# Kernel optimization log

Hardware: AMD Instinct MI355X
Metric: run time of the kernel (lower is better)

## Reference

```python
import jax, jax.numpy as jnp
from jax import lax
import numpy as np

DIM = 192
NH = 6
HEAD = DIM // NH
SCALE = HEAD ** -0.5
WS = (2, 7, 7)
NW = WS[0] * WS[1] * WS[2]  # 98 tokens per window
HID = 4 * DIM
EPS = 1e-5


def _rel_index():
    # static relative-position index, computed once in numpy
    cd, ch, cw = [np.arange(s) for s in WS]
    coords = np.stack(np.meshgrid(cd, ch, cw, indexing='ij')).reshape(3, -1)  # [3, NW]
    rel = coords[:, :, None] - coords[:, None, :]          # [3, NW, NW]
    rel = rel.transpose(1, 2, 0) + np.array([WS[0] - 1, WS[1] - 1, WS[2] - 1])
    rel[:, :, 0] *= (2 * WS[1] - 1) * (2 * WS[2] - 1)
    rel[:, :, 1] *= (2 * WS[2] - 1)
    return jnp.asarray(rel.sum(-1))                         # [NW, NW] int32

REL_IDX = _rel_index()


def _ln(x, g, b):
    mu = jnp.mean(x, -1, keepdims=True)
    var = jnp.mean(jnp.square(x - mu), -1, keepdims=True)
    return (x - mu) * lax.rsqrt(var + EPS) * g + b


def setup_inputs() -> dict:
    key = jax.random.key(0)
    ks = jax.random.split(key, 10)
    B, D, H, W = 2, 16, 56, 56
    N = D * H * W
    s = 0.02
    return {
        'x': jax.random.normal(ks[0], (B, N, DIM), jnp.float32),
        'norm1_g': jnp.ones((DIM,), jnp.float32),
        'norm1_b': jnp.zeros((DIM,), jnp.float32),
        'qkv_w': jax.random.normal(ks[1], (DIM, 3 * DIM), jnp.float32) * s,
        'qkv_b': jnp.zeros((3 * DIM,), jnp.float32),
        'bias_table': jax.random.normal(ks[2], ((2 * WS[0] - 1) * (2 * WS[1] - 1) * (2 * WS[2] - 1), NH), jnp.float32) * s,
        'proj_w': jax.random.normal(ks[3], (DIM, DIM), jnp.float32) * s,
        'proj_b': jnp.zeros((DIM,), jnp.float32),
        'norm2_g': jnp.ones((DIM,), jnp.float32),
        'norm2_b': jnp.zeros((DIM,), jnp.float32),
        'fc1_w': jax.random.normal(ks[4], (DIM, HID), jnp.float32) * s,
        'fc1_b': jnp.zeros((HID,), jnp.float32),
        'dw_w': jax.random.normal(ks[5], (HID, 1, 3, 3, 3), jnp.float32) * s,  # OIDHW depthwise
        'dw_b': jnp.zeros((HID,), jnp.float32),
        'fc2_w': jax.random.normal(ks[6], (HID, DIM), jnp.float32) * s,
        'fc2_b': jnp.zeros((DIM,), jnp.float32),
        'D': D, 'H': H, 'W': W,
    }


def reference(x, norm1_g, norm1_b, qkv_w, qkv_b, bias_table, proj_w, proj_b,
              norm2_g, norm2_b, fc1_w, fc1_b, dw_w, dw_b, fc2_w, fc2_b, D, H, W):
    B, N, C = x.shape
    Wd, Wh, Ww = WS
    nd, nh, nw = D // Wd, H // Wh, W // Ww

    # --- windowed attention branch ---
    h = _ln(x, norm1_g, norm1_b).reshape(B, D, H, W, C)
    h = h.reshape(B, nd, Wd, nh, Wh, nw, Ww, C)
    h = h.transpose(0, 1, 3, 5, 2, 4, 6, 7).reshape(-1, NW, C)  # [Bw, NW, C]
    Bw = h.shape[0]

    qkv = (h @ qkv_w + qkv_b).reshape(Bw, NW, 3, NH, HEAD)
    qkv = qkv.transpose(2, 0, 3, 1, 4)                           # [3, Bw, NH, NW, HEAD]
    q, k, v = qkv[0] * SCALE, qkv[1], qkv[2]

    attn = jnp.einsum('bhnd,bhmd->bhnm', q, k)                   # [Bw, NH, NW, NW]
    rel_bias = bias_table[REL_IDX]                               # [NW, NW, NH]
    attn = attn + rel_bias.transpose(2, 0, 1)[None]
    attn = jax.nn.softmax(attn, axis=-1)

    o = jnp.einsum('bhnm,bhmd->bhnd', attn, v)                   # [Bw, NH, NW, HEAD]
    o = o.transpose(0, 2, 1, 3).reshape(Bw, NW, C)
    o = o @ proj_w + proj_b

    # window reverse
    o = o.reshape(B, nd, nh, nw, Wd, Wh, Ww, C)
    o = o.transpose(0, 1, 4, 2, 5, 3, 6, 7).reshape(B, N, C)

    x = x + 0.5 * o  # DropPath scale_residual=0.5 in eval

    # --- MixFFN3D branch ---
    h = _ln(x, norm2_g, norm2_b)
    h = h @ fc1_w + fc1_b                                        # [B, N, HID]
    h = h.transpose(0, 2, 1).reshape(B, HID, D, H, W)
    h = lax.conv_general_dilated(
        h, dw_w, window_strides=(1, 1, 1), padding=[(1, 1)] * 3,
        dimension_numbers=('NCDHW', 'OIDHW', 'NCDHW'),
        feature_group_count=HID) + dw_b[None, :, None, None, None]
    h = h.reshape(B, HID, N).transpose(0, 2, 1)
    h = jax.nn.gelu(h, approximate=False)
    h = h @ fc2_w + fc2_b

    return x + 0.5 * h
```

## Files before the change

kernel.cpp:

```cpp
#include <hip/hip_runtime.h>
#include <hip/hip_bf16.h>

typedef unsigned short u16;
typedef unsigned int   u32;
typedef __bf16 bf16x8 __attribute__((ext_vector_type(8)));
typedef float  f32x4  __attribute__((ext_vector_type(4)));
typedef float  f32x2  __attribute__((ext_vector_type(2)));

#define M_TOK 100352
#define M_HALF 50176
#define DIMC  192
#define HIDC  768
#define SCALE_F 0.17677669529663688f

__device__ __forceinline__ float b2f(u16 u) {
    u32 x = ((u32)u) << 16; float f; __builtin_memcpy(&f, &x, 4); return f;
}
__device__ __forceinline__ u16 f2b(float f) {
    u32 x; __builtin_memcpy(&x, &f, 4);
    x = x + 0x7FFFu + ((x >> 16) & 1u);
    return (u16)(x >> 16);
}
__device__ __forceinline__ float lo2f(u32 w) {
    u32 x = w << 16; float f; __builtin_memcpy(&f, &x, 4); return f;
}
__device__ __forceinline__ float hi2f(u32 w) {
    u32 x = w & 0xFFFF0000u; float f; __builtin_memcpy(&f, &x, 4); return f;
}
__device__ __forceinline__ void g2l16(const u16* g, u16* l) {
    __builtin_amdgcn_global_load_lds(
        (const __attribute__((address_space(1))) u32*)g,
        (__attribute__((address_space(3))) u32*)l, 16, 0, 0);
}

__global__ __launch_bounds__(256) void prep_weights(
    const float* __restrict__ qkv_w, const float* __restrict__ proj_w,
    const float* __restrict__ fc1_w, const float* __restrict__ fc2_w,
    const float* __restrict__ dw_w,
    u16* __restrict__ qkvt, u16* __restrict__ projt, u16* __restrict__ fc1t,
    u16* __restrict__ fc2t, float* __restrict__ dwtf)
{
    int id = blockIdx.x * 256 + threadIdx.x;
    if (id < 110592)      { int n = id / 192, k = id % 192;                 qkvt[id] = f2b(qkv_w[k * 576 + n]); }
    else if (id < 147456) { int e = id - 110592, n = e / 192, k = e % 192;  projt[e] = f2b(proj_w[k * 192 + n]); }
    else if (id < 294912) { int e = id - 147456, n = e / 192, k = e % 192;  fc1t[e]  = f2b(fc1_w[k * 768 + n]); }
    else if (id < 442368) { int e = id - 294912, n = e / 768, k = e % 768;  fc2t[e]  = f2b(fc2_w[k * 192 + n]); }
    else if (id < 463104) { int e = id - 442368, t = e / 768, c = e % 768;  dwtf[e]  = dw_w[c * 27 + t]; }
}

__global__ __launch_bounds__(256) void biasmat_kernel(
    const float* __restrict__ btab, float* __restrict__ bmat)
{
    int id = blockIdx.x * 256 + threadIdx.x;
    if (id >= 6 * 112 * 112) return;
    int h = id / 12544, rem = id % 12544, i = rem / 112, j = rem % 112;
    float v;
    if (j >= 98)      v = -1e30f;
    else if (i >= 98) v = 0.0f;
    else {
        int di = i / 49, hi = (i / 7) % 7, wi = i % 7;
        int dj = j / 49, hj = (j / 7) % 7, wj = j % 7;
        int idx = (di - dj + 1) * 169 + (hi - hj + 6) * 13 + (wi - wj + 6);
        v = btab[idx * 6 + h];
    }
    bmat[id] = v;
}

template<bool PERM, bool BF_IN>
__global__ __launch_bounds__(256) void ln_kernel(
    const void* __restrict__ xin, const float* __restrict__ g,
    const float* __restrict__ bb, u16* __restrict__ out)
{
    int row  = blockIdx.x * 4 + (threadIdx.x >> 6);
    int lane = threadIdx.x & 63;
    float v0, v1, v2;
    if (BF_IN) {
        const u16* xr = (const u16*)xin + (size_t)row * DIMC;
        v0 = b2f(xr[lane]); v1 = b2f(xr[lane + 64]); v2 = b2f(xr[lane + 128]);
    } else {
        const float* xr = (const float*)xin + (size_t)row * DIMC;
        v0 = xr[lane]; v1 = xr[lane + 64]; v2 = xr[lane + 128];
    }
    float s  = v0 + v1 + v2;
    float s2 = v0 * v0 + v1 * v1 + v2 * v2;
    #pragma unroll
    for (int m = 1; m < 64; m <<= 1) { s += __shfl_xor(s, m); s2 += __shfl_xor(s2, m); }
    float mu = s * (1.0f / 192.0f);
    float rs = rsqrtf(s2 * (1.0f / 192.0f) - mu * mu + 1e-5f);
    size_t ob;
    if (PERM) {
        int b = row / 50176, r = row % 50176;
        int d = r / 3136, r2 = r % 3136, h = r2 / 56, w = r2 % 56;
        int widx = ((b * 8 + (d >> 1)) * 8 + h / 7) * 8 + w / 7;
        int tok  = (d & 1) * 49 + (h % 7) * 7 + (w % 7);
        ob = ((size_t)widx * 98 + tok) * DIMC;
    } else {
        ob = (size_t)row * DIMC;
    }
    out[ob + lane]       = f2b((v0 - mu) * rs * g[lane]       + bb[lane]);
    out[ob + lane + 64]  = f2b((v1 - mu) * rs * g[lane + 64]  + bb[lane + 64]);
    out[ob + lane + 128] = f2b((v2 - mu) * rs * g[lane + 128] + bb[lane + 128]);
}

template<int EPI>
__global__ __launch_bounds__(256) void gemm_bt(
    const u16* __restrict__ A, const u16* __restrict__ Bt,
    const float* __restrict__ bias, int K, int N, int NBN,
    u16* __restrict__ outb, const float* __restrict__ xres,
    u16* __restrict__ x2b, float* __restrict__ outf, int mofs)
{
    __shared__ __align__(16) u16 Alds[128 * 32];
    __shared__ __align__(16) u16 Blds[64 * 32];
    int bid = blockIdx.x;
    int cpx = gridDim.x >> 3;
    int swz = (bid & 7) * cpx + (bid >> 3);
    int m0 = (swz / NBN) * 128;
    int n0 = (swz % NBN) * 64;
    int t  = threadIdx.x;
    int ar = t >> 2, ac = (t & 3) * 8;
    int lane = t & 63, wid = t >> 6;
    int wm = wid >> 1, wn = wid & 1;
    int lrow = lane & 15, lko = (lane >> 4) * 8;
    const u16* Ag  = A  + (size_t)(m0 + ar) * K + ac;
    const u16* Ag2 = Ag + (size_t)64 * K;
    const u16* Bg  = Bt + (size_t)(n0 + ar) * K + ac;
    u16* lA  = Alds + t * 8;
    u16* lA2 = Alds + 2048 + t * 8;
    u16* lB  = Blds + t * 8;
    f32x4 acc[4][2] = {};
    for (int kt = 0; kt < K; kt += 32) {
        __syncthreads();
        g2l16(Ag  + kt, lA);
        g2l16(Ag2 + kt, lA2);
        g2l16(Bg  + kt, lB);
        __syncthreads();
        bf16x8 af[4], bfr[2];
        #pragma unroll
        for (int mi = 0; mi < 4; mi++)
            af[mi] = *(const bf16x8*)&Alds[(wm * 64 + mi * 16 + lrow) * 32 + lko];
        #pragma unroll
        for (int ni = 0; ni < 2; ni++)
            bfr[ni] = *(const bf16x8*)&Blds[(wn * 32 + ni * 16 + lrow) * 32 + lko];
        #pragma unroll
        for (int mi = 0; mi < 4; mi++)
            #pragma unroll
            for (int ni = 0; ni < 2; ni++)
                acc[mi][ni] = __builtin_amdgcn_mfma_f32_16x16x32_bf16(af[mi], bfr[ni], acc[mi][ni], 0, 0, 0);
    }
    int r0 = (lane >> 4) * 4, cl = lane & 15;
    #pragma unroll
    for (int ni = 0; ni < 2; ni++) {
        int col = n0 + wn * 32 + ni * 16 + cl;
        float bv = bias[col];
        #pragma unroll
        for (int mi = 0; mi < 4; mi++) {
            #pragma unroll
            for (int r = 0; r < 4; r++) {
                int row = m0 + wm * 64 + mi * 16 + r0 + r;
                float v = acc[mi][ni][r] + bv;
                if (EPI == 0) {
                    outb[(size_t)row * N + col] = f2b(v);
                } else if (EPI == 1) {
                    int widx = row / 98, tok = row % 98;
                    int b = widx >> 9, rem = widx & 511;
                    int bd = rem >> 6, bh = (rem >> 3) & 7, bw = rem & 7;
                    int td = tok / 49, rr = tok % 49, th = rr / 7, tw = rr % 7;
                    int d = bd * 2 + td, h = bh * 7 + th, w = bw * 7 + tw;
                    size_t gg = ((size_t)b * 50176 + (d * 56 + h) * 56 + w) * (size_t)N + col;
                    x2b[gg] = f2b(xres[gg] + 0.5f * v);
                } else {
                    size_t gg = (size_t)(row + mofs) * N + col;
                    outf[gg] = b2f(x2b[gg]) + 0.5f * v;
                }
            }
        }
    }
}

__global__ __launch_bounds__(64) void attn_mfma_kernel(
    const u16* __restrict__ qkv, const float* __restrict__ bmat,
    u16* __restrict__ outb)
{
    __shared__ __align__(16) u16 Klds[112 * 40];
    __shared__ __align__(16) u16 Vt[32 * 136];
    __shared__ __align__(16) u16 Plds[16 * 136];
    int widx = blockIdx.x, head = blockIdx.y;
    int l = threadIdx.x;
    int c = l & 15, g = l >> 4;
    size_t wbase = (size_t)widx * (98 * 576) + head * 32;

    for (int e = l; e < 448; e += 64) {
        int rr = e >> 2, seg = (e & 3) * 8;
        uint4 kr = {0, 0, 0, 0}, vr = {0, 0, 0, 0};
        if (rr < 98) {
            kr = *(const uint4*)(qkv + wbase + (size_t)rr * 576 + 192 + seg);
            vr = *(const uint4*)(qkv + wbase + (size_t)rr * 576 + 384 + seg);
        }
        *(uint4*)&Klds[rr * 40 + seg] = kr;
        int sw = ((seg >> 3) & 3) << 4;
        int pc = rr ^ sw;
        const u16* vp = (const u16*)&vr;
        #pragma unroll
        for (int u = 0; u < 8; u++)
            Vt[(seg + u) * 136 + pc] = vp[u];
    }
    {
        int d = l >> 1, half = l & 1;
        int sw = ((d >> 3) & 3) << 4;
        uint4 z = {0, 0, 0, 0};
        *(uint4*)&Vt[d * 136 + ((112 + 8 * half) ^ sw)] = z;
        if (l < 32) {
            int i = l >> 1; half = l & 1;
            int swp = ((i >> 2) & 3) << 4;
            *(uint4*)&Plds[i * 136 + ((112 + 8 * half) ^ swp)] = z;
        }
    }

    for (int it = 0; it < 7; ++it) {
        int qtok = 16 * it + c; if (qtok > 97) qtok = 97;
        bf16x8 qf = *(const bf16x8*)(qkv + wbase + (size_t)qtok * 576 + g * 8);
        f32x4 s[7];
        f32x4 z = {};
        #pragma unroll
        for (int jt = 0; jt < 7; ++jt) {
            bf16x8 kf = *(const bf16x8*)&Klds[(16 * jt + c) * 40 + g * 8];
            s[jt] = __builtin_amdgcn_mfma_f32_16x16x32_bf16(qf, kf, z, 0, 0, 0);
        }
        const float* bb = bmat + ((size_t)head * 112 + 16 * it + 4 * g) * 112 + c;
        float sm[4];
        #pragma unroll
        for (int r = 0; r < 4; ++r) {
            float m = -1e30f;
            #pragma unroll
            for (int jt = 0; jt < 7; ++jt) {
                float v = s[jt][r] * SCALE_F + bb[r * 112 + 16 * jt];
                s[jt][r] = v;
                m = fmaxf(m, v);
            }
            m = fmaxf(m, __shfl_xor(m, 1)); m = fmaxf(m, __shfl_xor(m, 2));
            m = fmaxf(m, __shfl_xor(m, 4)); m = fmaxf(m, __shfl_xor(m, 8));
            float su = 0.f;
            #pragma unroll
            for (int jt = 0; jt < 7; ++jt) {
                float p = __expf(s[jt][r] - m);
                s[jt][r] = p;
                su += p;
            }
            su += __shfl_xor(su, 1); su += __shfl_xor(su, 2);
            su += __shfl_xor(su, 4); su += __shfl_xor(su, 8);
            sm[r] = su;
        }
        #pragma unroll
        for (int r = 0; r < 4; ++r) {
            int prow = 4 * g + r;
            int swp = ((prow >> 2) & 3) << 4;
            #pragma unroll
            for (int jt = 0; jt < 7; ++jt)
                Plds[prow * 136 + ((16 * jt + c) ^ swp)] = f2b(s[jt][r]);
        }
        bf16x8 pa[4];
        int swr = ((c >> 2) & 3) << 4;
        #pragma unroll
        for (int ks = 0; ks < 4; ++ks)
            pa[ks] = *(const bf16x8*)&Plds[c * 136 + ((32 * ks + 8 * g) ^ swr)];
        #pragma unroll
        for (int dt = 0; dt < 2; ++dt) {
            f32x4 o = {};
            int vrow = 16 * dt + c;
            int swv = ((vrow >> 3) & 3) << 4;
            #pragma unroll
            for (int ks = 0; ks < 4; ++ks) {
                bf16x8 vb = *(const bf16x8*)&Vt[vrow * 136 + ((32 * ks + 8 * g) ^ swv)];
                o = __builtin_amdgcn_mfma_f32_16x16x32_bf16(pa[ks], vb, o, 0, 0, 0);
            }
            #pragma unroll
            for (int r = 0; r < 4; ++r) {
                int row = 16 * it + 4 * g + r;
                if (row < 98)
                    outb[((size_t)widx * 98 + row) * DIMC + head * 32 + 16 * dt + c]
                        = f2b(o[r] / sm[r]);
            }
        }
    }
}

__global__ __launch_bounds__(256, 8) void dwconv_gelu_kernel(
    const u16* __restrict__ hid, const float* __restrict__ dwtf,
    const float* __restrict__ dwb, u16* __restrict__ outb)
{
    int bid = blockIdx.x;
    int swz = (bid & 7) * 1176 + (bid >> 3);
    int gid = swz * 256 + threadIdx.x;
    int cg = gid % 192;
    int t  = gid / 192;
    int d  = t & 15;
    t >>= 4;
    int wg = t % 14;
    int h  = t / 14;
    int w0 = wg * 4;
    int c0 = cg * 4;

    f32x2 acc[4][2];
    {
        float4 bv = *(const float4*)(dwb + c0);
        #pragma unroll
        for (int wi = 0; wi < 4; ++wi) {
            acc[wi][0] = f32x2{bv.x, bv.y};
            acc[wi][1] = f32x2{bv.z, bv.w};
        }
    }

    #pragma unroll
    for (int iz = 0; iz < 3; ++iz) {
        int zz = d - 1 + iz;
        if ((unsigned)zz >= 16u) continue;
        #pragma unroll
        for (int iy = 0; iy < 3; ++iy) {
            int yy = h - 1 + iy;
            if ((unsigned)yy >= 56u) continue;
            uint2 raw[6];
            const u16* rp = hid + ((size_t)(zz * 56 + yy) * 56 + w0 - 1) * HIDC + c0;
            #pragma unroll
            for (int ix = 0; ix < 6; ++ix) {
                uint2 iv = {0, 0};
                if ((unsigned)(w0 - 1 + ix) < 56u)
                    iv = *(const uint2*)(rp + (size_t)ix * HIDC);
                raw[ix] = iv;
            }
            const float* wrow = dwtf + (size_t)(iz * 9 + iy * 3) * HIDC + c0;
            float4 wv0 = *(const float4*)(wrow);
            float4 wv1 = *(const float4*)(wrow + HIDC);
            float4 wv2 = *(const float4*)(wrow + 2 * HIDC);
            f32x2 wp[3][2] = {
                { f32x2{wv0.x, wv0.y}, f32x2{wv0.z, wv0.w} },
                { f32x2{wv1.x, wv1.y}, f32x2{wv1.z, wv1.w} },
                { f32x2{wv2.x, wv2.y}, f32x2{wv2.z, wv2.w} } };
            #pragma unroll
            for (int p = 0; p < 6; ++p) {
                f32x2 i0 = f32x2{lo2f(raw[p].x), hi2f(raw[p].x)};
                f32x2 i1 = f32x2{lo2f(raw[p].y), hi2f(raw[p].y)};
                #pragma unroll
                for (int dx = 0; dx < 3; ++dx) {
                    if (dx > p || dx < p - 3) continue;
                    acc[p - dx][0] += i0 * wp[dx][0];
                    acc[p - dx][1] += i1 * wp[dx][1];
                }
            }
        }
    }

    size_t tok0 = (size_t)(d * 56 + h) * 56 + w0;
    #pragma unroll
    for (int wi = 0; wi < 4; ++wi) {
        u16 res[4];
        #pragma unroll
        for (int pr = 0; pr < 2; ++pr) {
            #pragma unroll
            for (int u = 0; u < 2; ++u) {
                float a = acc[wi][pr][u];
                float tt = a * (1.5957691216f + 0.0713548162f * a * a);
                res[pr * 2 + u] = f2b(a / (1.0f + __expf(-tt)));
            }
        }
        uint2 ov;
        ov.x = (u32)res[0] | ((u32)res[1] << 16);
        ov.y = (u32)res[2] | ((u32)res[3] << 16);
        *(uint2*)(outb + (tok0 + wi) * HIDC + c0) = ov;
    }
}

extern "C" void kernel_launch(void* const* d_in, const int* in_sizes, int n_in,
                              void* d_out, int out_size, void* d_ws, size_t ws_size,
                              hipStream_t stream)
{
    const float* x      = (const float*)d_in[0];
    const float* n1g    = (const float*)d_in[1];
    const float* n1b    = (const float*)d_in[2];
    const float* qkv_w  = (const float*)d_in[3];
    const float* qkv_b  = (const float*)d_in[4];
    const float* btab   = (const float*)d_in[5];
    const float* proj_w = (const float*)d_in[6];
    const float* proj_b = (const float*)d_in[7];
    const float* n2g    = (const float*)d_in[8];
    const float* n2b    = (const float*)d_in[9];
    const float* fc1_w  = (const float*)d_in[10];
    const float* fc1_b  = (const float*)d_in[11];
    const float* dw_w   = (const float*)d_in[12];
    const float* dw_b   = (const float*)d_in[13];
    const float* fc2_w  = (const float*)d_in[14];
    const float* fc2_b  = (const float*)d_in[15];

    char* ws = (char*)d_ws;
    u16*   qkvt  = (u16*)(ws);
    u16*   projt = (u16*)(ws + 221184);
    u16*   fc1t  = (u16*)(ws + 294912);
    u16*   fc2t  = (u16*)(ws + 589824);
    float* dwtf  = (float*)(ws + 884736);
    u16*   r1    = (u16*)(ws + 1160192);
    u16*   qkvb  = (u16*)(ws + 39695360LL);
    u16*   x2b   = (u16*)(ws + 39695360LL);
    u16*   hid_c = (u16*)(ws + 78230528LL);
    float* bmat  = (float*)(ws + 155300864LL);
    u16*   gelu_c= (u16*)(ws + 155300864LL);

    prep_weights<<<dim3(1809), dim3(256), 0, stream>>>(qkv_w, proj_w, fc1_w, fc2_w, dw_w,
                                                       qkvt, projt, fc1t, fc2t, dwtf);
    biasmat_kernel<<<dim3(294), dim3(256), 0, stream>>>(btab, bmat);
    ln_kernel<true, false><<<dim3(25088), dim3(256), 0, stream>>>(x, n1g, n1b, r1);
    gemm_bt<0><<<dim3(7056), dim3(256), 0, stream>>>(r1, qkvt, qkv_b, 192, 576, 9,
                                                     qkvb, nullptr, nullptr, nullptr, 0);
    attn_mfma_kernel<<<dim3(1024, 6), dim3(64), 0, stream>>>(qkvb, bmat, r1);
    gemm_bt<1><<<dim3(2352), dim3(256), 0, stream>>>(r1, projt, proj_b, 192, 192, 3,
                                                     nullptr, x, x2b, nullptr, 0);
    ln_kernel<false, true><<<dim3(25088), dim3(256), 0, stream>>>(x2b, n2g, n2b, r1);
    for (int b = 0; b < 2; b++) {
        const u16* h2c = r1 + (size_t)b * M_HALF * DIMC;
        gemm_bt<0><<<dim3(4704), dim3(256), 0, stream>>>(h2c, fc1t, fc1_b, 192, 768, 12,
                                                         hid_c, nullptr, nullptr, nullptr, 0);
        dwconv_gelu_kernel<<<dim3(9408), dim3(256), 0, stream>>>(hid_c, dwtf, dw_b, gelu_c);
        gemm_bt<2><<<dim3(1176), dim3(256), 0, stream>>>(gelu_c, fc2t, fc2_b, 768, 192, 3,
                                                         nullptr, nullptr, x2b, (float*)d_out,
                                                         b * M_HALF);
    }
}
```

Before: 728.9 us.

## Split dwconv into interior/edge kernels and double GEMM k-step per sync

The GEMM loop now loads 64 K-columns per iteration (two 32-wide LDS slices) and runs two MFMA sub-steps between barriers, halving the number of __syncthreads per tile. The depthwise conv+GELU is split into an interior kernel with all boundary checks removed and a separate edge kernel that keeps the checks for boundary tokens. This trims barrier and branch overhead at the cost of doubled LDS use in the GEMM and an extra launch. The GEMM change assumes K is a multiple of 64, which holds for 192 and 768.

```diff
diff --git a/kernel.cpp b/kernel.cpp
--- a/kernel.cpp
+++ b/kernel.cpp
@@ -109,43 +109,47 @@
     u16* __restrict__ outb, const float* __restrict__ xres,
     u16* __restrict__ x2b, float* __restrict__ outf, int mofs)
 {
-    __shared__ __align__(16) u16 Alds[128 * 32];
-    __shared__ __align__(16) u16 Blds[64 * 32];
+    __shared__ __align__(16) u16 Alds[2 * 128 * 32];
+    __shared__ __align__(16) u16 Blds[2 * 64 * 32];
     int bid = blockIdx.x;
     int cpx = gridDim.x >> 3;
     int swz = (bid & 7) * cpx + (bid >> 3);
     int m0 = (swz / NBN) * 128;
     int n0 = (swz % NBN) * 64;
     int t  = threadIdx.x;
-    int ar = t >> 2, ac = (t & 3) * 8;
     int lane = t & 63, wid = t >> 6;
     int wm = wid >> 1, wn = wid & 1;
     int lrow = lane & 15, lko = (lane >> 4) * 8;
-    const u16* Ag  = A  + (size_t)(m0 + ar) * K + ac;
-    const u16* Ag2 = Ag + (size_t)64 * K;
-    const u16* Bg  = Bt + (size_t)(n0 + ar) * K + ac;
-    u16* lA  = Alds + t * 8;
-    u16* lA2 = Alds + 2048 + t * 8;
-    u16* lB  = Blds + t * 8;
+    int sr = t >> 2, sc = (t & 3) * 8;
+    const u16* Ag = A  + (size_t)(m0 + sr) * K + sc;
+    const u16* Bg = Bt + (size_t)(n0 + sr) * K + sc;
+    u16* lA = Alds + t * 8;
+    u16* lB = Blds + t * 8;
     f32x4 acc[4][2] = {};
-    for (int kt = 0; kt < K; kt += 32) {
+    for (int kt = 0; kt < K; kt += 64) {
         __syncthreads();
-        g2l16(Ag  + kt, lA);
-        g2l16(Ag2 + kt, lA2);
-        g2l16(Bg  + kt, lB);
+        g2l16(Ag + kt,                    lA);
+        g2l16(Ag + (size_t)64 * K + kt,   lA + 2048);
+        g2l16(Ag + kt + 32,               lA + 4096);
+        g2l16(Ag + (size_t)64 * K + kt + 32, lA + 6144);
+        g2l16(Bg + kt,      lB);
+        g2l16(Bg + kt + 32, lB + 2048);
         __syncthreads();
-        bf16x8 af[4], bfr[2];
-        #pragma unroll
-        for (int mi = 0; mi < 4; mi++)
-            af[mi] = *(const bf16x8*)&Alds[(wm * 64 + mi * 16 + lrow) * 32 + lko];
-        #pragma unroll
-        for (int ni = 0; ni < 2; ni++)
-            bfr[ni] = *(const bf16x8*)&Blds[(wn * 32 + ni * 16 + lrow) * 32 + lko];
-        #pragma unroll
-        for (int mi = 0; mi < 4; mi++)
+        #pragma unroll
+        for (int kk = 0; kk < 2; ++kk) {
+            bf16x8 af[4], bfr[2];
+            #pragma unroll
+            for (int mi = 0; mi < 4; mi++)
+                af[mi] = *(const bf16x8*)&Alds[kk * 4096 + (wm * 64 + mi * 16 + lrow) * 32 + lko];
             #pragma unroll
             for (int ni = 0; ni < 2; ni++)
-                acc[mi][ni] = __builtin_amdgcn_mfma_f32_16x16x32_bf16(af[mi], bfr[ni], acc[mi][ni], 0, 0, 0);
+                bfr[ni] = *(const bf16x8*)&Blds[kk * 2048 + (wn * 32 + ni * 16 + lrow) * 32 + lko];
+            #pragma unroll
+            for (int mi = 0; mi < 4; mi++)
+                #pragma unroll
+                for (int ni = 0; ni < 2; ni++)
+                    acc[mi][ni] = __builtin_amdgcn_mfma_f32_16x16x32_bf16(af[mi], bfr[ni], acc[mi][ni], 0, 0, 0);
+        }
     }
     int r0 = (lane >> 4) * 4, cl = lane & 15;
     #pragma unroll
@@ -284,20 +288,21 @@
     }
 }
 
-__global__ __launch_bounds__(256, 8) void dwconv_gelu_kernel(
+__global__ __launch_bounds__(256, 8) void dwconv_gelu_int(
     const u16* __restrict__ hid, const float* __restrict__ dwtf,
     const float* __restrict__ dwb, u16* __restrict__ outb)
 {
     int bid = blockIdx.x;
-    int swz = (bid & 7) * 1176 + (bid >> 3);
+    int xcd = bid & 7, lin = bid >> 3;
+    int swz = (xcd < 4 ? xcd * 851 : 3404 + (xcd - 4) * 850) + lin;
     int gid = swz * 256 + threadIdx.x;
     int cg = gid % 192;
-    int t  = gid / 192;
-    int d  = t & 15;
-    t >>= 4;
-    int wg = t % 14;
-    int h  = t / 14;
-    int w0 = wg * 4;
+    int iu = gid / 192;
+    int d  = iu % 14 + 1;
+    int r  = iu / 14;
+    int wg = r % 12;
+    int h  = r / 12 + 1;
+    int w0 = wg * 4 + 4;
     int c0 = cg * 4;
 
     f32x2 acc[4][2];
@@ -310,24 +315,18 @@
         }
     }
 
+    const u16* rp0 = hid + (((size_t)(d - 1) * 56 + (h - 1)) * 56 + (w0 - 1)) * HIDC + c0;
+    const float* wb0 = dwtf + c0;
     #pragma unroll
     for (int iz = 0; iz < 3; ++iz) {
-        int zz = d - 1 + iz;
-        if ((unsigned)zz >= 16u) continue;
         #pragma unroll
         for (int iy = 0; iy < 3; ++iy) {
-            int yy = h - 1 + iy;
-            if ((unsigned)yy >= 56u) continue;
+            const u16* rp = rp0 + (size_t)(iz * 3136 + iy * 56) * HIDC;
             uint2 raw[6];
-            const u16* rp = hid + ((size_t)(zz * 56 + yy) * 56 + w0 - 1) * HIDC + c0;
-            #pragma unroll
-            for (int ix = 0; ix < 6; ++ix) {
-                uint2 iv = {0, 0};
-                if ((unsigned)(w0 - 1 + ix) < 56u)
-                    iv = *(const uint2*)(rp + (size_t)ix * HIDC);
-                raw[ix] = iv;
-            }
-            const float* wrow = dwtf + (size_t)(iz * 9 + iy * 3) * HIDC + c0;
+            #pragma unroll
+            for (int ix = 0; ix < 6; ++ix)
+                raw[ix] = *(const uint2*)(rp + (size_t)ix * HIDC);
+            const float* wrow = wb0 + (size_t)(iz * 9 + iy * 3) * HIDC;
             float4 wv0 = *(const float4*)(wrow);
             float4 wv1 = *(const float4*)(wrow + HIDC);
             float4 wv2 = *(const float4*)(wrow + 2 * HIDC);
@@ -354,14 +353,95 @@
     for (int wi = 0; wi < 4; ++wi) {
         u16 res[4];
         #pragma unroll
-        for (int pr = 0; pr < 2; ++pr) {
+        for (int pr = 0; pr < 2; ++pr)
             #pragma unroll
             for (int u = 0; u < 2; ++u) {
                 float a = acc[wi][pr][u];
                 float tt = a * (1.5957691216f + 0.0713548162f * a * a);
                 res[pr * 2 + u] = f2b(a / (1.0f + __expf(-tt)));
             }
-        }
+        uint2 ov;
+        ov.x = (u32)res[0] | ((u32)res[1] << 16);
+        ov.y = (u32)res[2] | ((u32)res[3] << 16);
+        *(uint2*)(outb + (tok0 + wi) * HIDC + c0) = ov;
+    }
+}
+
+__global__ __launch_bounds__(256, 8) void dwconv_gelu_edge(
+    const u16* __restrict__ hid, const float* __restrict__ dwtf,
+    const float* __restrict__ dwb, u16* __restrict__ outb)
+{
+    int gid = blockIdx.x * 256 + threadIdx.x;
+    int cg = gid % 192;
+    int u  = gid / 192;
+    int d, h, wg;
+    if (u < 1568)      { d = (u < 784) ? 0 : 15; int rr = u % 784; h = rr / 14; wg = rr % 14; }
+    else if (u < 1960) { int rr = u - 1568; h = (rr < 196) ? 0 : 55; rr %= 196; d = 1 + rr / 14; wg = rr % 14; }
+    else               { int rr = u - 1960; wg = (rr < 756) ? 0 : 13; rr %= 756; d = 1 + rr / 54; h = 1 + rr % 54; }
+    int w0 = wg * 4;
+    int c0 = cg * 4;
+
+    f32x2 acc[4][2];
+    {
+        float4 bv = *(const float4*)(dwb + c0);
+        #pragma unroll
+        for (int wi = 0; wi < 4; ++wi) {
+            acc[wi][0] = f32x2{bv.x, bv.y};
+            acc[wi][1] = f32x2{bv.z, bv.w};
+        }
+    }
+
+    #pragma unroll
+    for (int iz = 0; iz < 3; ++iz) {
+        int zz = d - 1 + iz;
+        if ((unsigned)zz >= 16u) continue;
+        #pragma unroll
+        for (int iy = 0; iy < 3; ++iy) {
+            int yy = h - 1 + iy;
+            if ((unsigned)yy >= 56u) continue;
+            uint2 raw[6];
+            const u16* rp = hid + ((size_t)(zz * 56 + yy) * 56 + w0 - 1) * HIDC + c0;
+            #pragma unroll
+            for (int ix = 0; ix < 6; ++ix) {
+                uint2 iv = {0, 0};
+                if ((unsigned)(w0 - 1 + ix) < 56u)
+                    iv = *(const uint2*)(rp + (size_t)ix * HIDC);
+                raw[ix] = iv;
+            }
+            const float* wrow = dwtf + (size_t)(iz * 9 + iy * 3) * HIDC + c0;
+            float4 wv0 = *(const float4*)(wrow);
+            float4 wv1 = *(const float4*)(wrow + HIDC);
+            float4 wv2 = *(const float4*)(wrow + 2 * HIDC);
+            f32x2 wp[3][2] = {
+                { f32x2{wv0.x, wv0.y}, f32x2{wv0.z, wv0.w} },
+                { f32x2{wv1.x, wv1.y}, f32x2{wv1.z, wv1.w} },
+                { f32x2{wv2.x, wv2.y}, f32x2{wv2.z, wv2.w} } };
+            #pragma unroll
+            for (int p = 0; p < 6; ++p) {
+                f32x2 i0 = f32x2{lo2f(raw[p].x), hi2f(raw[p].x)};
+                f32x2 i1 = f32x2{lo2f(raw[p].y), hi2f(raw[p].y)};
+                #pragma unroll
+                for (int dx = 0; dx < 3; ++dx) {
+                    if (dx > p || dx < p - 3) continue;
+                    acc[p - dx][0] += i0 * wp[dx][0];
+                    acc[p - dx][1] += i1 * wp[dx][1];
+                }
+            }
+        }
+    }
+
+    size_t tok0 = (size_t)(d * 56 + h) * 56 + w0;
+    #pragma unroll
+    for (int wi = 0; wi < 4; ++wi) {
+        u16 res[4];
+        #pragma unroll
+        for (int pr = 0; pr < 2; ++pr)
+            #pragma unroll
+            for (int u2 = 0; u2 < 2; ++u2) {
+                float a = acc[wi][pr][u2];
+                float tt = a * (1.5957691216f + 0.0713548162f * a * a);
+                res[pr * 2 + u2] = f2b(a / (1.0f + __expf(-tt)));
+            }
         uint2 ov;
         ov.x = (u32)res[0] | ((u32)res[1] << 16);
         ov.y = (u32)res[2] | ((u32)res[3] << 16);
@@ -417,7 +497,8 @@
         const u16* h2c = r1 + (size_t)b * M_HALF * DIMC;
         gemm_bt<0><<<dim3(4704), dim3(256), 0, stream>>>(h2c, fc1t, fc1_b, 192, 768, 12,
                                                          hid_c, nullptr, nullptr, nullptr, 0);
-        dwconv_gelu_kernel<<<dim3(9408), dim3(256), 0, stream>>>(hid_c, dwtf, dw_b, gelu_c);
+        dwconv_gelu_int<<<dim3(6804), dim3(256), 0, stream>>>(hid_c, dwtf, dw_b, gelu_c);
+        dwconv_gelu_edge<<<dim3(2604), dim3(256), 0, stream>>>(hid_c, dwtf, dw_b, gelu_c);
         gemm_bt<2><<<dim3(1176), dim3(256), 0, stream>>>(gelu_c, fc2t, fc2_b, 768, 192, 3,
                                                          nullptr, nullptr, x2b, (float*)d_out,
                                                          b * M_HALF);
```

New measurement: 905.9 us. 24.3% more time.
